# Kernel optimization log

Hardware: AMD Instinct MI355X
Metric: run time of the kernel (lower is better)

The kernel has to match this reference:

```python
import jax, jax.numpy as jnp
import numpy as np

H = W = 2048
TANH_C = 1.1486328125  # probability-correction constant from the model
DEG2RAD = np.float32(np.pi / 180.0)

# Fire-spread direction angle (degrees, East=0, counterclockwise) from the
# neighbor at 3x3 window position (r, c) toward the center cell.
DIR_DEG = jnp.array([[315., 270., 225.],
                     [  0.,   0., 180.],
                     [ 45.,  90., 135.]], dtype=jnp.float32)
CENTER_MASK = jnp.ones((3, 3), jnp.float32).at[1, 1].set(0.0)  # exclude self


def _neighborhood(x):
    """x: [H,W] -> [H,W,3,3] with [i,j,r,c] = x[i+r-1, j+c-1], zero padded."""
    xp = jnp.pad(x, 1)
    return jnp.stack(
        [jnp.stack([xp[r:r + H, c:c + W] for c in range(3)], axis=-1)
         for r in range(3)], axis=-2)


def setup_inputs() -> dict:
    key = jax.random.key(0)
    ks = jax.random.split(key, 8)
    p_veg = jax.random.uniform(ks[0], (H, W), jnp.float32)
    p_den = jax.random.uniform(ks[1], (H, W), jnp.float32)
    wind_velocity = jax.random.uniform(ks[2], (H, W), jnp.float32) * 10.0
    wind_towards_direction = jax.random.uniform(ks[3], (H, W), jnp.float32) * 360.0
    slope = (jax.random.uniform(ks[4], (H, W, 3, 3), jnp.float32) - 0.5) * 60.0
    burning = jax.random.uniform(ks[5], (H, W)) < 0.01  # sparse initial ignition
    burned = jnp.zeros((H, W), dtype=bool)
    rand_ignite = jax.random.uniform(ks[6], (H, W), jnp.float32)
    rand_continue = jax.random.uniform(ks[7], (H, W), jnp.float32)
    return dict(
        p_veg=p_veg, p_den=p_den,
        wind_velocity=wind_velocity, wind_towards_direction=wind_towards_direction,
        slope=slope,
        a=jnp.float32(0.1), p_h=jnp.float32(0.3),
        c_1=jnp.float32(0.1), c_2=jnp.float32(0.1), p_continue=jnp.float32(0.3),
        rand_ignite=rand_ignite, rand_continue=rand_continue,
        burning=burning, burned=burned,
    )


def reference(p_veg, p_den, wind_velocity, wind_towards_direction, slope,
              a, p_h, c_1, c_2, p_continue,
              rand_ignite, rand_continue, burning, burned):
    # p_w = exp(c1*V) * exp(c2*V*(cos(theta_w)-1)), theta_w = angle between
    # wind direction and per-neighbor spread direction. [H,W,3,3]
    theta_w = (wind_towards_direction[..., None, None] - DIR_DEG) * DEG2RAD
    p_w = (jnp.exp(c_1 * wind_velocity)[..., None, None]
           * jnp.exp(c_2 * wind_velocity[..., None, None] * (jnp.cos(theta_w) - 1.0)))
    # p_s = exp(a * theta_s), slope angle in radians. [H,W,3,3]
    p_s = jnp.exp(a * slope * DEG2RAD)
    # p_propagate = tanh(c * p_h*(1+p_veg)*(1+p_den)*p_w*p_s)
    p_base = p_h * (1.0 + p_veg) * (1.0 + p_den)  # [H,W]
    p_prop = jnp.tanh(TANH_C * (p_base[..., None, None] * p_w * p_s))
    # 8-neighbor burning indicators (center masked out). [H,W,3,3]
    nbr_burning = _neighborhood(burning.astype(jnp.float32)) * CENTER_MASK
    # p_ignite = 1 - prod_j (1 - p_propagate_j * burning_j)
    p_ignite = 1.0 - jnp.prod(1.0 - p_prop * nbr_burning, axis=(-2, -1))
    # Stochastic state transition.
    burnable = ~burning & ~burned
    new_ignited = burnable & (rand_ignite < p_ignite)
    keep = burning & (rand_continue < p_continue)
    new_burning = new_ignited | keep
    new_burned = burned | (burning & ~keep)
    return p_ignite, jnp.stack([new_burning, new_burned])
```

## Files before the change

kernel.cpp:

```cpp
#include <hip/hip_runtime.h>
#include <math.h>

namespace {

constexpr int H = 2048;
constexpr int W = 2048;
constexpr int HW = H * W;
constexpr float TANH_C  = 1.1486328125f;
constexpr float DEG2RAD = 0.017453292519943295f;
constexpr float RT2H    = 0.70710678118654752f;
constexpr float LOG2E   = 1.4426950408889634f;
constexpr float TWOPI   = 6.283185307179586f;

__device__ __forceinline__ float fexp2(float x) {
#if __has_builtin(__builtin_amdgcn_exp2f)
    return __builtin_amdgcn_exp2f(x);
#else
    return __exp2f(x);
#endif
}
__device__ __forceinline__ float fcos_rev(float x) {
#if __has_builtin(__builtin_amdgcn_cosf)
    return __builtin_amdgcn_cosf(x);
#else
    return __cosf(x * TWOPI);
#endif
}
__device__ __forceinline__ float fsin_rev(float x) {
#if __has_builtin(__builtin_amdgcn_sinf)
    return __builtin_amdgcn_sinf(x);
#else
    return __sinf(x * TWOPI);
#endif
}
__device__ __forceinline__ float frcp(float x) {
#if __has_builtin(__builtin_amdgcn_rcpf)
    return __builtin_amdgcn_rcpf(x);
#else
    return 1.0f / x;
#endif
}

__global__ __launch_bounds__(256) void wildfire_step(
    const float* __restrict__ p_veg,  const float* __restrict__ p_den,
    const float* __restrict__ wind_v, const float* __restrict__ wind_d,
    const float* __restrict__ slope,
    const float* __restrict__ s_a,  const float* __restrict__ s_ph,
    const float* __restrict__ s_c1, const float* __restrict__ s_c2,
    const float* __restrict__ s_pc,
    const float* __restrict__ rand_ig, const float* __restrict__ rand_co,
    const int* __restrict__ burning, const int* __restrict__ burned,
    float* __restrict__ out)
{
    __shared__ __align__(16) float sb[3][1032];
    const int t  = (int)threadIdx.x;
    const int i  = (int)blockIdx.y;
    const int j0 = (int)blockIdx.x * 1024;

    for (int r = 0; r < 3; ++r) {
        const int ii = i + r - 1;
        for (int c = t; c < 1026; c += 256) {
            const int jj = j0 - 1 + c;
            float v = 0.f;
            if (ii >= 0 && ii < H && jj >= 0 && jj < W)
                v = burning[ii * W + jj] ? 1.f : 0.f;
            sb[r][c] = v;
        }
    }
    __syncthreads();

    const int jb  = t * 4;
    const int idx = i * W + j0 + jb;

    float r0[8], r1[8], r2[8];
    {
        const float4 a0 = *reinterpret_cast<const float4*>(&sb[0][jb]);
        const float4 a1 = *reinterpret_cast<const float4*>(&sb[0][jb + 4]);
        const float4 b0 = *reinterpret_cast<const float4*>(&sb[1][jb]);
        const float4 b1 = *reinterpret_cast<const float4*>(&sb[1][jb + 4]);
        const float4 c0 = *reinterpret_cast<const float4*>(&sb[2][jb]);
        const float4 c1 = *reinterpret_cast<const float4*>(&sb[2][jb + 4]);
        r0[0]=a0.x; r0[1]=a0.y; r0[2]=a0.z; r0[3]=a0.w; r0[4]=a1.x; r0[5]=a1.y; r0[6]=a1.z; r0[7]=a1.w;
        r1[0]=b0.x; r1[1]=b0.y; r1[2]=b0.z; r1[3]=b0.w; r1[4]=b1.x; r1[5]=b1.y; r1[6]=b1.z; r1[7]=b1.w;
        r2[0]=c0.x; r2[1]=c0.y; r2[2]=c0.z; r2[3]=c0.w; r2[4]=c1.x; r2[5]=c1.y; r2[6]=c1.z; r2[7]=c1.w;
    }

    float anyn[4], pig[4];
    bool  isb[4], ni[4];
#pragma unroll
    for (int x = 0; x < 4; ++x) {
        anyn[x] = ((r0[x] + r0[x+1]) + (r0[x+2] + r1[x]))
                + ((r1[x+2] + r2[x]) + (r2[x+1] + r2[x+2]));
        isb[x]  = (r1[x+1] != 0.f);
        pig[x]  = 0.f;
        ni[x]   = false;
    }

    const int4  burned4 = *reinterpret_cast<const int4*>(burned + idx);
    const int   bn[4]   = {burned4.x, burned4.y, burned4.z, burned4.w};
    const float p_cont  = s_pc[0];

    float rc[4] = {0.f, 0.f, 0.f, 0.f};
    if (isb[0] || isb[1] || isb[2] || isb[3]) {
        const float4 rco4 = *reinterpret_cast<const float4*>(rand_co + idx);
        rc[0]=rco4.x; rc[1]=rco4.y; rc[2]=rco4.z; rc[3]=rco4.w;
    }

    if ((anyn[0] + anyn[1] + anyn[2] + anyn[3]) != 0.f) {
        const float a_  = s_a[0];
        const float p_h = s_ph[0];
        const float c1  = s_c1[0];
        const float c2  = s_c2[0];

        const float4 pv4  = *reinterpret_cast<const float4*>(p_veg  + idx);
        const float4 pd4  = *reinterpret_cast<const float4*>(p_den  + idx);
        const float4 wv4  = *reinterpret_cast<const float4*>(wind_v + idx);
        const float4 wd4  = *reinterpret_cast<const float4*>(wind_d + idx);
        const float4 rig4 = *reinterpret_cast<const float4*>(rand_ig + idx);
        const float pv[4]  = {pv4.x, pv4.y, pv4.z, pv4.w};
        const float pd[4]  = {pd4.x, pd4.y, pd4.z, pd4.w};
        const float wv[4]  = {wv4.x, wv4.y, wv4.z, wv4.w};
        const float wd[4]  = {wd4.x, wd4.y, wd4.z, wd4.w};
        const float rig[4] = {rig4.x, rig4.y, rig4.z, rig4.w};

        float sl[36];
        __builtin_memcpy(sl, slope + (size_t)idx * 9, 36 * sizeof(float));

        const float aslL = (a_ * DEG2RAD) * LOG2E;

#pragma unroll
        for (int x = 0; x < 4; ++x) {
            if (anyn[x] != 0.f) {
                const float wrev = wd[x] * (1.f / 360.f);
                const float cw = fcos_rev(wrev);
                const float sw = fsin_rev(wrev);

                const float Lc2wv = (LOG2E * c2) * wv[x];
                const float cwv = Lc2wv * cw, swv = Lc2wv * sw;
                const float cwr = RT2H * cwv, swr = RT2H * swv;
                const float dpl = cwr + swr;
                const float dmi = cwr - swr;
                const float p_base = (p_h * (1.f + pv[x])) * (1.f + pd[x]);
                const float Cz2 = (2.f * LOG2E * TANH_C) * p_base
                                * fexp2(LOG2E * (c1 * wv[x] - c2 * wv[x]));
                const float* s = sl + 9 * x;

#define NEIGHBOR(K, b, T, sv)                                            \
                const float q##K = fmaf(aslL, (sv), (T));                \
                const float z##K = Cz2 * fexp2(q##K);                    \
                const float E##K = fexp2(z##K);                          \
                const float d##K = fmaf((b), E##K, 1.f);

                NEIGHBOR(0, r0[x],    dmi, s[0])
                NEIGHBOR(1, r0[x+1], -swv, s[1])
                NEIGHBOR(2, r0[x+2], -dpl, s[2])
                NEIGHBOR(3, r1[x],    cwv, s[3])
                NEIGHBOR(5, r1[x+2], -cwv, s[5])
                NEIGHBOR(6, r2[x],    dpl, s[6])
                NEIGHBOR(7, r2[x+1],  swv, s[7])
                NEIGHBOR(8, r2[x+2], -dmi, s[8])
#undef NEIGHBOR
                const float den = ((d0 * d1) * (d2 * d3)) * ((d5 * d6) * (d7 * d8));
                const float num = fexp2(anyn[x]);
                pig[x] = fmaf(-num, frcp(den), 1.f);

                ni[x] = (!isb[x]) && (bn[x] == 0) && (rig[x] < pig[x]);
            }
        }
    }

    float4 o0, o1, o2;
    float* o0p = &o0.x; float* o1p = &o1.x; float* o2p = &o2.x;
#pragma unroll
    for (int x = 0; x < 4; ++x) {
        const bool keep = isb[x] && (rc[x] < p_cont);
        const bool nb   = ni[x] || keep;
        const bool nd   = (bn[x] != 0) || (isb[x] && !keep);
        o0p[x] = pig[x];
        o1p[x] = nb ? 1.f : 0.f;
        o2p[x] = nd ? 1.f : 0.f;
    }
    *reinterpret_cast<float4*>(out + idx)          = o0;
    *reinterpret_cast<float4*>(out + HW + idx)     = o1;
    *reinterpret_cast<float4*>(out + 2 * HW + idx) = o2;
}

}

extern "C" void kernel_launch(void* const* d_in, const int* in_sizes, int n_in,
                              void* d_out, int out_size, void* d_ws, size_t ws_size,
                              hipStream_t stream)
{
    (void)in_sizes; (void)n_in; (void)out_size; (void)d_ws; (void)ws_size;
    dim3 grid(W / 1024, H, 1);
    dim3 block(256, 1, 1);
    hipLaunchKernelGGL(wildfire_step, grid, block, 0, stream,
        (const float*)d_in[0],  (const float*)d_in[1],
        (const float*)d_in[2],  (const float*)d_in[3],
        (const float*)d_in[4],
        (const float*)d_in[5],  (const float*)d_in[6],
        (const float*)d_in[7],  (const float*)d_in[8],
        (const float*)d_in[9],
        (const float*)d_in[10], (const float*)d_in[11],
        (const int*)d_in[12],   (const int*)d_in[13],
        (float*)d_out);
}
```

Before: 317.7 us.

## Compact active cells into an LDS queue to balance sparse neighbor work

Each block now collects the cells that have at least one burning neighbor into a shared-memory queue with an LDS atomic. Threads then process that queue densely, one cell per thread, and write p_ignite into LDS for the final output pass. This replaces per-thread 4-cell branches that diverged within a wavefront. The burning-row load also becomes vectorised int4 with separate halo cells. The cost is an extra barrier, LDS atomics, and scalar gathers of inputs and slope for the queued cells in place of float4 loads.

```diff
diff --git a/kernel.cpp b/kernel.cpp
--- a/kernel.cpp
+++ b/kernel.cpp
@@ -53,128 +53,146 @@
     float* __restrict__ out)
 {
     __shared__ __align__(16) float sb[3][1032];
+    __shared__ __align__(16) float pig_lds[1024];
+    __shared__ unsigned short q[1024];
+    __shared__ int qn;
+
     const int t  = (int)threadIdx.x;
     const int i  = (int)blockIdx.y;
     const int j0 = (int)blockIdx.x * 1024;
+    const int rowbase = i * W + j0;
+
+    if (t == 0) qn = 0;
 
     for (int r = 0; r < 3; ++r) {
         const int ii = i + r - 1;
-        for (int c = t; c < 1026; c += 256) {
-            const int jj = j0 - 1 + c;
-            float v = 0.f;
-            if (ii >= 0 && ii < H && jj >= 0 && jj < W)
-                v = burning[ii * W + jj] ? 1.f : 0.f;
-            sb[r][c] = v;
-        }
+        const bool rowok = (ii >= 0) && (ii < H);
+        int4 v = make_int4(0, 0, 0, 0);
+        if (rowok)
+            v = *reinterpret_cast<const int4*>(burning + ii * W + j0 + 4 * t);
+        float4 f;
+        f.x = v.x ? 1.f : 0.f;  f.y = v.y ? 1.f : 0.f;
+        f.z = v.z ? 1.f : 0.f;  f.w = v.w ? 1.f : 0.f;
+        *reinterpret_cast<float4*>(&sb[r][4 + 4 * t]) = f;
+        if (t == 0)
+            sb[r][3] = (rowok && j0 > 0) ?
+                       (burning[ii * W + j0 - 1] ? 1.f : 0.f) : 0.f;
+        if (t == 1)
+            sb[r][4 + 1024] = (rowok && j0 + 1024 < W) ?
+                       (burning[ii * W + j0 + 1024] ? 1.f : 0.f) : 0.f;
     }
     __syncthreads();
 
-    const int jb  = t * 4;
-    const int idx = i * W + j0 + jb;
-
-    float r0[8], r1[8], r2[8];
+    const int jb = t * 4;
+    const int idx = rowbase + jb;
+
+    float r0[6], r1[6], r2[6];
     {
-        const float4 a0 = *reinterpret_cast<const float4*>(&sb[0][jb]);
-        const float4 a1 = *reinterpret_cast<const float4*>(&sb[0][jb + 4]);
-        const float4 b0 = *reinterpret_cast<const float4*>(&sb[1][jb]);
-        const float4 b1 = *reinterpret_cast<const float4*>(&sb[1][jb + 4]);
-        const float4 c0 = *reinterpret_cast<const float4*>(&sb[2][jb]);
-        const float4 c1 = *reinterpret_cast<const float4*>(&sb[2][jb + 4]);
-        r0[0]=a0.x; r0[1]=a0.y; r0[2]=a0.z; r0[3]=a0.w; r0[4]=a1.x; r0[5]=a1.y; r0[6]=a1.z; r0[7]=a1.w;
-        r1[0]=b0.x; r1[1]=b0.y; r1[2]=b0.z; r1[3]=b0.w; r1[4]=b1.x; r1[5]=b1.y; r1[6]=b1.z; r1[7]=b1.w;
-        r2[0]=c0.x; r2[1]=c0.y; r2[2]=c0.z; r2[3]=c0.w; r2[4]=c1.x; r2[5]=c1.y; r2[6]=c1.z; r2[7]=c1.w;
-    }
-
-    float anyn[4], pig[4];
-    bool  isb[4], ni[4];
+        const float4 a = *reinterpret_cast<const float4*>(&sb[0][4 + jb]);
+        const float4 b = *reinterpret_cast<const float4*>(&sb[1][4 + jb]);
+        const float4 c = *reinterpret_cast<const float4*>(&sb[2][4 + jb]);
+        r0[0] = sb[0][3 + jb]; r0[1] = a.x; r0[2] = a.y; r0[3] = a.z; r0[4] = a.w; r0[5] = sb[0][8 + jb];
+        r1[0] = sb[1][3 + jb]; r1[1] = b.x; r1[2] = b.y; r1[3] = b.z; r1[4] = b.w; r1[5] = sb[1][8 + jb];
+        r2[0] = sb[2][3 + jb]; r2[1] = c.x; r2[2] = c.y; r2[3] = c.z; r2[4] = c.w; r2[5] = sb[2][8 + jb];
+    }
+
+    float anyn[4];
+    bool  isb[4];
 #pragma unroll
     for (int x = 0; x < 4; ++x) {
         anyn[x] = ((r0[x] + r0[x+1]) + (r0[x+2] + r1[x]))
                 + ((r1[x+2] + r2[x]) + (r2[x+1] + r2[x+2]));
         isb[x]  = (r1[x+1] != 0.f);
-        pig[x]  = 0.f;
-        ni[x]   = false;
-    }
-
-    const int4  burned4 = *reinterpret_cast<const int4*>(burned + idx);
-    const int   bn[4]   = {burned4.x, burned4.y, burned4.z, burned4.w};
-    const float p_cont  = s_pc[0];
-
-    float rc[4] = {0.f, 0.f, 0.f, 0.f};
-    if (isb[0] || isb[1] || isb[2] || isb[3]) {
-        const float4 rco4 = *reinterpret_cast<const float4*>(rand_co + idx);
-        rc[0]=rco4.x; rc[1]=rco4.y; rc[2]=rco4.z; rc[3]=rco4.w;
-    }
-
-    if ((anyn[0] + anyn[1] + anyn[2] + anyn[3]) != 0.f) {
+        if (anyn[x] != 0.f) {
+            const int pos = atomicAdd(&qn, 1);
+            q[pos] = (unsigned short)(jb + x);
+        }
+    }
+    *reinterpret_cast<float4*>(&pig_lds[jb]) = make_float4(0.f, 0.f, 0.f, 0.f);
+    __syncthreads();
+
+    const int n = qn;
+    for (int k = t; k < n; k += 256) {
+        const int cell = (int)q[k];
+        const int c    = 4 + cell;
+        const float b0 = sb[0][c-1], b1 = sb[0][c], b2 = sb[0][c+1];
+        const float b3 = sb[1][c-1],                b5 = sb[1][c+1];
+        const float b6 = sb[2][c-1], b7 = sb[2][c], b8 = sb[2][c+1];
+        const float cnt = ((b0 + b1) + (b2 + b3)) + ((b5 + b6) + (b7 + b8));
+
+        const int gidx = rowbase + cell;
+        const float pv = p_veg[gidx];
+        const float pd = p_den[gidx];
+        const float wv = wind_v[gidx];
+        const float wd = wind_d[gidx];
+        float sl[9];
+        __builtin_memcpy(sl, slope + (size_t)gidx * 9, 9 * sizeof(float));
+
         const float a_  = s_a[0];
         const float p_h = s_ph[0];
         const float c1  = s_c1[0];
         const float c2  = s_c2[0];
 
-        const float4 pv4  = *reinterpret_cast<const float4*>(p_veg  + idx);
-        const float4 pd4  = *reinterpret_cast<const float4*>(p_den  + idx);
-        const float4 wv4  = *reinterpret_cast<const float4*>(wind_v + idx);
-        const float4 wd4  = *reinterpret_cast<const float4*>(wind_d + idx);
+        const float wrev = wd * (1.f / 360.f);
+        const float cw = fcos_rev(wrev);
+        const float sw = fsin_rev(wrev);
+
+        const float Lc2wv = (LOG2E * c2) * wv;
+        const float cwv = Lc2wv * cw, swv = Lc2wv * sw;
+        const float cwr = RT2H * cwv, swr = RT2H * swv;
+        const float dpl = cwr + swr;
+        const float dmi = cwr - swr;
+        const float aslL = (a_ * DEG2RAD) * LOG2E;
+        const float p_base = (p_h * (1.f + pv)) * (1.f + pd);
+        const float Cz2 = (2.f * LOG2E * TANH_C) * p_base
+                        * fexp2(LOG2E * (c1 * wv - c2 * wv));
+
+#define NEIGHBOR(K, b, T, sv)                                            \
+        const float q##K = fmaf(aslL, (sv), (T));                        \
+        const float z##K = Cz2 * fexp2(q##K);                            \
+        const float E##K = fexp2(z##K);                                  \
+        const float d##K = fmaf((b), E##K, 1.f);
+
+        NEIGHBOR(0, b0,  dmi, sl[0])
+        NEIGHBOR(1, b1, -swv, sl[1])
+        NEIGHBOR(2, b2, -dpl, sl[2])
+        NEIGHBOR(3, b3,  cwv, sl[3])
+        NEIGHBOR(5, b5, -cwv, sl[5])
+        NEIGHBOR(6, b6,  dpl, sl[6])
+        NEIGHBOR(7, b7,  swv, sl[7])
+        NEIGHBOR(8, b8, -dmi, sl[8])
+#undef NEIGHBOR
+        const float den = ((d0 * d1) * (d2 * d3)) * ((d5 * d6) * (d7 * d8));
+        const float num = fexp2(cnt);
+        pig_lds[cell] = fmaf(-num, frcp(den), 1.f);
+    }
+    __syncthreads();
+
+    const int4  burned4 = *reinterpret_cast<const int4*>(burned + idx);
+    const int   bn[4]   = {burned4.x, burned4.y, burned4.z, burned4.w};
+    const float p_cont  = s_pc[0];
+
+    const float4 pig4 = *reinterpret_cast<const float4*>(&pig_lds[jb]);
+    const float pig[4] = {pig4.x, pig4.y, pig4.z, pig4.w};
+
+    float rc[4] = {1.f, 1.f, 1.f, 1.f};
+    if (isb[0] || isb[1] || isb[2] || isb[3]) {
+        const float4 rco4 = *reinterpret_cast<const float4*>(rand_co + idx);
+        rc[0] = rco4.x; rc[1] = rco4.y; rc[2] = rco4.z; rc[3] = rco4.w;
+    }
+    float rig[4] = {1.f, 1.f, 1.f, 1.f};
+    if ((anyn[0] + anyn[1]) + (anyn[2] + anyn[3]) != 0.f) {
         const float4 rig4 = *reinterpret_cast<const float4*>(rand_ig + idx);
-        const float pv[4]  = {pv4.x, pv4.y, pv4.z, pv4.w};
-        const float pd[4]  = {pd4.x, pd4.y, pd4.z, pd4.w};
-        const float wv[4]  = {wv4.x, wv4.y, wv4.z, wv4.w};
-        const float wd[4]  = {wd4.x, wd4.y, wd4.z, wd4.w};
-        const float rig[4] = {rig4.x, rig4.y, rig4.z, rig4.w};
-
-        float sl[36];
-        __builtin_memcpy(sl, slope + (size_t)idx * 9, 36 * sizeof(float));
-
-        const float aslL = (a_ * DEG2RAD) * LOG2E;
-
-#pragma unroll
-        for (int x = 0; x < 4; ++x) {
-            if (anyn[x] != 0.f) {
-                const float wrev = wd[x] * (1.f / 360.f);
-                const float cw = fcos_rev(wrev);
-                const float sw = fsin_rev(wrev);
-
-                const float Lc2wv = (LOG2E * c2) * wv[x];
-                const float cwv = Lc2wv * cw, swv = Lc2wv * sw;
-                const float cwr = RT2H * cwv, swr = RT2H * swv;
-                const float dpl = cwr + swr;
-                const float dmi = cwr - swr;
-                const float p_base = (p_h * (1.f + pv[x])) * (1.f + pd[x]);
-                const float Cz2 = (2.f * LOG2E * TANH_C) * p_base
-                                * fexp2(LOG2E * (c1 * wv[x] - c2 * wv[x]));
-                const float* s = sl + 9 * x;
-
-#define NEIGHBOR(K, b, T, sv)                                            \
-                const float q##K = fmaf(aslL, (sv), (T));                \
-                const float z##K = Cz2 * fexp2(q##K);                    \
-                const float E##K = fexp2(z##K);                          \
-                const float d##K = fmaf((b), E##K, 1.f);
-
-                NEIGHBOR(0, r0[x],    dmi, s[0])
-                NEIGHBOR(1, r0[x+1], -swv, s[1])
-                NEIGHBOR(2, r0[x+2], -dpl, s[2])
-                NEIGHBOR(3, r1[x],    cwv, s[3])
-                NEIGHBOR(5, r1[x+2], -cwv, s[5])
-                NEIGHBOR(6, r2[x],    dpl, s[6])
-                NEIGHBOR(7, r2[x+1],  swv, s[7])
-                NEIGHBOR(8, r2[x+2], -dmi, s[8])
-#undef NEIGHBOR
-                const float den = ((d0 * d1) * (d2 * d3)) * ((d5 * d6) * (d7 * d8));
-                const float num = fexp2(anyn[x]);
-                pig[x] = fmaf(-num, frcp(den), 1.f);
-
-                ni[x] = (!isb[x]) && (bn[x] == 0) && (rig[x] < pig[x]);
-            }
-        }
+        rig[0] = rig4.x; rig[1] = rig4.y; rig[2] = rig4.z; rig[3] = rig4.w;
     }
 
     float4 o0, o1, o2;
     float* o0p = &o0.x; float* o1p = &o1.x; float* o2p = &o2.x;
 #pragma unroll
     for (int x = 0; x < 4; ++x) {
+        const bool ni   = (!isb[x]) && (bn[x] == 0) && (rig[x] < pig[x]);
         const bool keep = isb[x] && (rc[x] < p_cont);
-        const bool nb   = ni[x] || keep;
+        const bool nb   = ni || keep;
         const bool nd   = (bn[x] != 0) || (isb[x] && !keep);
         o0p[x] = pig[x];
         o1p[x] = nb ? 1.f : 0.f;
```

Result: faster. 305.2 us (-3.9%).
